# Optimization experiments

Hardware: AMD Instinct MI355X
Metric: run time of the kernel (lower is better)

## Reference

```python
import jax, jax.numpy as jnp
import numpy as np
import math

B, C, A, W, H = 8, 128, 16, 64, 64


def setup_inputs() -> dict:
    key = jax.random.key(0)
    ks = jax.random.split(key, 7)
    s_in = 1.0 / math.sqrt(C)
    return {
        "x": jax.random.normal(ks[0], (B, C, W, H), dtype=jnp.float32),
        "Wq": jax.random.normal(ks[1], (A, C), dtype=jnp.float32) * s_in,
        "bq": jnp.zeros((A,), dtype=jnp.float32),
        "Wk": jax.random.normal(ks[2], (A, C), dtype=jnp.float32) * s_in,
        "bk": jnp.zeros((A,), dtype=jnp.float32),
        "Wv": jax.random.normal(ks[3], (C, C), dtype=jnp.float32) * s_in,
        "bv": jnp.zeros((C,), dtype=jnp.float32),
    }


def reference(x, Wq, bq, Wk, bk, Wv, bv):
    # 1x1 convs == per-pixel linear projections
    q = jnp.einsum('ac,bcwh->bawh', Wq, x) + bq[None, :, None, None]  # [B,A,W,H]
    k = jnp.einsum('ac,bcwh->bawh', Wk, x) + bk[None, :, None, None]  # [B,A,W,H]
    v = jnp.einsum('vc,bcwh->bvwh', Wv, x) + bv[None, :, None, None]  # [B,C,W,H]

    scale = 1.0 / math.sqrt(q.shape[1])
    # full spatial attention: [B, W, H, W, H]
    attn = jnp.einsum('bawh,baWH->bwhWH', q, k)
    b, w, h, _, _ = attn.shape
    attn = jax.nn.softmax(attn.reshape(b, w, h, -1) * scale, axis=-1)
    attn = attn.reshape(b, w, h, w, h)
    out = jnp.einsum('bwhWH,bvWH->bvwh', attn, v)  # [B,C,W,H]
    return out
```

## Files before the change

kernel.cpp:

```cpp
#include <hip/hip_runtime.h>
#include <math.h>

#define BB 8
#define CC 128
#define NN 4096

typedef _Float16 f16;
typedef _Float16 f16x4v __attribute__((ext_vector_type(4)));
typedef _Float16 f16x8 __attribute__((ext_vector_type(8)));
typedef float f32x16 __attribute__((ext_vector_type(16)));

#if __has_builtin(__builtin_amdgcn_exp2f)
#define EXP2(x) __builtin_amdgcn_exp2f(x)
#else
#define EXP2(x) __expf((x)*0.69314718056f)
#endif

#define QSCALE 0.360673760222f
#define SHIFT  5.770780163555f

#define WF_BYTES 65536

__global__ __launch_bounds__(256)
void prep_kernel(const float* __restrict__ Wq, const float* __restrict__ bq,
                 const float* __restrict__ Wk, const float* __restrict__ bk,
                 const float* __restrict__ Wv, const float* __restrict__ bv,
                 f16* __restrict__ Wf, float* __restrict__ biasS)
{
    const int tg = blockIdx.x*256 + threadIdx.x;
    if (tg < 2560) {
        const int mt = tg >> 9, ks = (tg >> 6) & 7, l = tg & 63;
        const int n32 = l & 31, h = l >> 5;
        const int r = mt*32 + n32;
        f16x8 v8;
        #pragma unroll
        for (int i = 0; i < 8; i++) {
            int c = ks*16 + 8*h + i;
            float wv_;
            if (r < 16)      wv_ = QSCALE * Wq[r*CC + c];
            else if (r < 32) wv_ = Wk[(r-16)*CC + c];
            else             wv_ = Wv[(r-32)*CC + c];
            v8[i] = (f16)wv_;
        }
        *(f16x8*)&Wf[(size_t)tg*8] = v8;
    }
    if (blockIdx.x == 0 && threadIdx.x < 160) {
        int r = threadIdx.x;
        biasS[r] = r < 16 ? QSCALE*bq[r] : (r < 32 ? bk[r-16] : bv[r-32]);
    }
}

__global__ __launch_bounds__(256)
void proj_kernel(const float* __restrict__ x, const f16* __restrict__ Wf,
                 const float* __restrict__ biasS,
                 f16* __restrict__ Qt, f16* __restrict__ Kt, f16* __restrict__ Vf)
{
    __shared__ __align__(16) f16 Vl[CC*140];

    const int tid  = threadIdx.x;
    const int lane = tid & 63;
    const int wv   = tid >> 6;
    const int b    = blockIdx.x & 7;
    const int pt   = blockIdx.x >> 3;
    const int n32  = lane & 31;
    const int half = lane >> 5;
    const int p    = pt*128 + wv*32 + n32;

    const float* xp = x + (size_t)b*CC*NN + p;
    f16x8 xf[8];
    #pragma unroll
    for (int ks = 0; ks < 8; ks++) {
        float xv[8];
        #pragma unroll
        for (int i = 0; i < 8; i++) xv[i] = xp[(size_t)(ks*16 + 8*half + i)*NN];
        #pragma unroll
        for (int i = 0; i < 8; i++) xf[ks][i] = (f16)xv[i];
    }

    f32x16 acc[5];
    #pragma unroll
    for (int mt = 0; mt < 5; mt++) acc[mt] = (f32x16)0.0f;
    #pragma unroll
    for (int ks = 0; ks < 8; ks++) {
        #pragma unroll
        for (int mt = 0; mt < 5; mt++) {
            f16x8 wfr = *(const f16x8*)&Wf[((size_t)(mt*8 + ks)*64 + lane)*8];
            acc[mt] = __builtin_amdgcn_mfma_f32_32x32x16_f16(wfr, xf[ks], acc[mt], 0, 0, 0);
        }
    }

    #pragma unroll
    for (int mt = 0; mt < 5; mt++) {
        #pragma unroll
        for (int q = 0; q < 4; q++) {
            float4 b4 = *(const float4*)&biasS[mt*32 + q*8 + 4*half];
            acc[mt][q*4+0] += b4.x; acc[mt][q*4+1] += b4.y;
            acc[mt][q*4+2] += b4.z; acc[mt][q*4+3] += b4.w;
        }
    }

    {
        size_t qkoff = ((size_t)b*NN + p)*16;
        f16x4v s0, s1, s2, s3;
        #pragma unroll
        for (int i = 0; i < 4; i++) {
            s0[i] = (f16)acc[0][i];    s1[i] = (f16)acc[0][4+i];
            s2[i] = (f16)acc[0][8+i];  s3[i] = (f16)acc[0][12+i];
        }
        *(f16x4v*)&Qt[qkoff + 4*half]     = s0;
        *(f16x4v*)&Qt[qkoff + 8 + 4*half] = s1;
        *(f16x4v*)&Kt[qkoff + 4*half]     = s2;
        *(f16x4v*)&Kt[qkoff + 8 + 4*half] = s3;
    }

    #pragma unroll
    for (int mt = 1; mt < 5; mt++) {
        #pragma unroll
        for (int g = 0; g < 16; g++) {
            int c = (mt-1)*32 + (g & 3) + 8*(g >> 2) + 4*half;
            Vl[c*140 + wv*32 + n32] = (f16)acc[mt][g];
        }
    }
    __syncthreads();

    #pragma unroll
    for (int pass = 0; pass < 8; pass++) {
        int item = pass*256 + tid;
        int l    = item & 63;
        int f    = (item >> 6) & 15;
        int ktl  = item >> 10;
        int kc   = f >> 2, ct = f & 3;
        int li   = l & 31, h2 = l >> 5;
        const f16* src = &Vl[(ct*32 + li)*140 + ktl*64 + kc*16 + 4*h2];
        f16x4v lo = *(const f16x4v*)&src[0];
        f16x4v hi = *(const f16x4v*)&src[8];
        f16x8 v8;
        #pragma unroll
        for (int i = 0; i < 4; i++) { v8[i] = lo[i]; v8[4+i] = hi[i]; }
        int ktg = pt*2 + ktl;
        *(f16x8*)&Vf[((((size_t)b*64 + ktg)*16 + f)*64 + l)*8] = v8;
    }
}

__global__ __launch_bounds__(256, 2)
void attn_kernel(const f16* __restrict__ Qt, const f16* __restrict__ Kt,
                 const f16* __restrict__ Vf, float* __restrict__ out)
{
    __shared__ __align__(16) unsigned char lds_raw[52480];

    const int tid  = threadIdx.x;
    const int lane = tid & 63;
    const int wv   = tid >> 6;
    const int b    = blockIdx.x & 7;
    const int qt   = blockIdx.x >> 3;
    const int q0   = qt*64;
    const int n32  = lane & 31;
    const int half = lane >> 5;

    const f16* vb = Vf + (size_t)b*64*16*512;
    const f16* kb = Kt + (size_t)b*NN*16;
    const f16x8 qfA = *(const f16x8*)&Qt[((size_t)b*NN + q0 + n32)*16 + half*8];
    const f16x8 qfB = *(const f16x8*)&Qt[((size_t)b*NN + q0 + 32 + n32)*16 + half*8];

    f32x16 ofA[4], ofB[4];
    #pragma unroll
    for (int ct = 0; ct < 4; ct++) { ofA[ct] = (f32x16)0.0f; ofB[ct] = (f32x16)0.0f; }
    float psA[4] = {0,0,0,0}, psB[4] = {0,0,0,0};

    f16x8 kf0 = *(const f16x8*)&kb[((size_t)wv*64 + n32)*16 + half*8];
    f16x8 kf1 = *(const f16x8*)&kb[((size_t)wv*64 + 32 + n32)*16 + half*8];

    for (int kt = wv; kt < NN/64; kt += 4) {
        const int ktn = (kt + 4 < NN/64) ? kt + 4 : kt;
        f16x8 kf0n = *(const f16x8*)&kb[((size_t)ktn*64 + n32)*16 + half*8];
        f16x8 kf1n = *(const f16x8*)&kb[((size_t)ktn*64 + 32 + n32)*16 + half*8];

        f32x16 St0 = __builtin_amdgcn_mfma_f32_32x32x16_f16(kf0, qfA, (f32x16)(-SHIFT), 0, 0, 0);
        f32x16 St1 = __builtin_amdgcn_mfma_f32_32x32x16_f16(kf1, qfA, (f32x16)(-SHIFT), 0, 0, 0);
        f32x16 St2 = __builtin_amdgcn_mfma_f32_32x32x16_f16(kf0, qfB, (f32x16)(-SHIFT), 0, 0, 0);
        f32x16 St3 = __builtin_amdgcn_mfma_f32_32x32x16_f16(kf1, qfB, (f32x16)(-SHIFT), 0, 0, 0);

        f16x8 pfA[4], pfB[4];
        #pragma unroll
        for (int g = 0; g < 16; g++) {
            float e0 = EXP2(St0[g]); psA[g & 3] += e0; pfA[(g >> 3)][g & 7]     = (f16)e0;
            float e1 = EXP2(St1[g]); psA[g & 3] += e1; pfA[2 + (g >> 3)][g & 7] = (f16)e1;
            float e2 = EXP2(St2[g]); psB[g & 3] += e2; pfB[(g >> 3)][g & 7]     = (f16)e2;
            float e3 = EXP2(St3[g]); psB[g & 3] += e3; pfB[2 + (g >> 3)][g & 7] = (f16)e3;
        }

        const f16* vt = vb + (size_t)kt*8192;
        #pragma unroll
        for (int kc = 0; kc < 4; kc++) {
            #pragma unroll
            for (int ct = 0; ct < 4; ct++) {
                f16x8 vfr = *(const f16x8*)&vt[((kc*4 + ct)*64 + lane)*8];
                ofA[ct] = __builtin_amdgcn_mfma_f32_32x32x16_f16(pfA[kc], vfr, ofA[ct], 0, 0, 0);
                ofB[ct] = __builtin_amdgcn_mfma_f32_32x32x16_f16(pfB[kc], vfr, ofB[ct], 0, 0, 0);
            }
        }
        kf0 = kf0n; kf1 = kf1n;
    }

    float lsA = (psA[0] + psA[1]) + (psA[2] + psA[3]);
    float lsB = (psB[0] + psB[1]) + (psB[2] + psB[3]);
    lsA += __shfl_xor(lsA, 32);
    lsB += __shfl_xor(lsB, 32);

    __syncthreads();
    if (wv != 0) {
        unsigned char* base = lds_raw + (size_t)(wv-1)*17408 + (size_t)lane*272;
        #pragma unroll
        for (int ct = 0; ct < 4; ct++) {
            #pragma unroll
            for (int h = 0; h < 2; h++) {
                f16x8 ta, tb;
                #pragma unroll
                for (int j = 0; j < 8; j++) { ta[j] = (f16)ofA[ct][h*8+j]; tb[j] = (f16)ofB[ct][h*8+j]; }
                *(f16x8*)(base + ct*32 + h*16)       = ta;
                *(f16x8*)(base + 128 + ct*32 + h*16) = tb;
            }
        }
        *(float*)(base + 256) = lsA;
        *(float*)(base + 260) = lsB;
    }
    __syncthreads();
    if (wv == 0) {
        #pragma unroll
        for (int s2 = 0; s2 < 3; s2++) {
            unsigned char* base = lds_raw + (size_t)s2*17408 + (size_t)lane*272;
            #pragma unroll
            for (int ct = 0; ct < 4; ct++) {
                #pragma unroll
                for (int h = 0; h < 2; h++) {
                    f16x8 ta = *(const f16x8*)(base + ct*32 + h*16);
                    f16x8 tb = *(const f16x8*)(base + 128 + ct*32 + h*16);
                    #pragma unroll
                    for (int j = 0; j < 8; j++) { ofA[ct][h*8+j] += (float)ta[j]; ofB[ct][h*8+j] += (float)tb[j]; }
                }
            }
            lsA += *(const float*)(base + 256);
            lsB += *(const float*)(base + 260);
        }
        float* ls_inv = (float*)(lds_raw + 52224);
        if (lane < 32) { ls_inv[lane] = 1.f / lsA; ls_inv[32 + lane] = 1.f / lsB; }
        float invA[16], invB[16];
        #pragma unroll
        for (int g = 0; g < 16; g++) {
            int row = (g & 3) + 8*(g >> 2) + 4*half;
            invA[g] = ls_inv[row];
            invB[g] = ls_inv[32 + row];
        }
        float* Tb = (float*)lds_raw;
        #pragma unroll
        for (int ct = 0; ct < 4; ct++) {
            #pragma unroll
            for (int g = 0; g < 16; g++) {
                int row = (g & 3) + 8*(g >> 2) + 4*half;
                Tb[(ct*32 + n32)*68 + row]      = ofA[ct][g] * invA[g];
                Tb[(ct*32 + n32)*68 + 32 + row] = ofB[ct][g] * invB[g];
            }
        }
    }
    __syncthreads();
    {
        const float* Tb = (const float*)lds_raw;
        #pragma unroll
        for (int it = 0; it < 8; it++) {
            int idx = it*256 + tid;
            int c = idx >> 4, qq = idx & 15;
            *(float4*)&out[((size_t)b*CC + c)*NN + q0 + qq*4] =
                *(const float4*)&Tb[c*68 + qq*4];
        }
    }
}

extern "C" void kernel_launch(void* const* d_in, const int* in_sizes, int n_in,
                              void* d_out, int out_size, void* d_ws, size_t ws_size,
                              hipStream_t stream) {
    const float* x  = (const float*)d_in[0];
    const float* Wq = (const float*)d_in[1];
    const float* bq = (const float*)d_in[2];
    const float* Wk = (const float*)d_in[3];
    const float* bk = (const float*)d_in[4];
    const float* Wv = (const float*)d_in[5];
    const float* bv = (const float*)d_in[6];
    float* out = (float*)d_out;

    f16* Qw = (f16*)d_ws;
    f16* Kw = Qw + (size_t)BB*NN*16;
    f16* Vw = Kw + (size_t)BB*NN*16;
    unsigned char* tail = (unsigned char*)d_out + (size_t)out_size*4 - WF_BYTES;
    f16*   Wf    = (f16*)tail;
    float* biasS = (float*)(tail + 49152);

    hipLaunchKernelGGL(prep_kernel, dim3(10), dim3(256), 0, stream,
                       Wq, bq, Wk, bk, Wv, bv, Wf, biasS);
    hipLaunchKernelGGL(proj_kernel, dim3(256), dim3(256), 0, stream,
                       x, Wf, biasS, Qw, Kw, Vw);
    hipLaunchKernelGGL(attn_kernel, dim3(512), dim3(256), 0, stream,
                       Qw, Kw, Vw, out);
}
```

Measured before the change: 154.8 us.

## Halve attention query tile to 32 rows, double grid, prefetch V fragments into registers

The attention kernel now processes 32 queries per block instead of 64 and launches 1024 blocks, which halves per-wave accumulator registers and LDS use and doubles the number of blocks. V fragments for the next key tile are prefetched into registers while the current tile's MFMAs run, hiding global load latency. The projection kernel's x loads become nontemporal. The cost is that each block now reads K and V for only half as many queries, so total K/V traffic doubles.

```diff
diff --git a/kernel.cpp b/kernel.cpp
--- a/kernel.cpp
+++ b/kernel.cpp
@@ -72,7 +72,8 @@
     for (int ks = 0; ks < 8; ks++) {
         float xv[8];
         #pragma unroll
-        for (int i = 0; i < 8; i++) xv[i] = xp[(size_t)(ks*16 + 8*half + i)*NN];
+        for (int i = 0; i < 8; i++)
+            xv[i] = __builtin_nontemporal_load(&xp[(size_t)(ks*16 + 8*half + i)*NN]);
         #pragma unroll
         for (int i = 0; i < 8; i++) xf[ks][i] = (f16)xv[i];
     }
@@ -146,119 +147,112 @@
 void attn_kernel(const f16* __restrict__ Qt, const f16* __restrict__ Kt,
                  const f16* __restrict__ Vf, float* __restrict__ out)
 {
-    __shared__ __align__(16) unsigned char lds_raw[52480];
+    __shared__ __align__(16) unsigned char lds_raw[27776];
 
     const int tid  = threadIdx.x;
     const int lane = tid & 63;
     const int wv   = tid >> 6;
     const int b    = blockIdx.x & 7;
     const int qt   = blockIdx.x >> 3;
-    const int q0   = qt*64;
+    const int q0   = qt*32;
     const int n32  = lane & 31;
     const int half = lane >> 5;
 
     const f16* vb = Vf + (size_t)b*64*16*512;
     const f16* kb = Kt + (size_t)b*NN*16;
-    const f16x8 qfA = *(const f16x8*)&Qt[((size_t)b*NN + q0 + n32)*16 + half*8];
-    const f16x8 qfB = *(const f16x8*)&Qt[((size_t)b*NN + q0 + 32 + n32)*16 + half*8];
-
-    f32x16 ofA[4], ofB[4];
-    #pragma unroll
-    for (int ct = 0; ct < 4; ct++) { ofA[ct] = (f32x16)0.0f; ofB[ct] = (f32x16)0.0f; }
-    float psA[4] = {0,0,0,0}, psB[4] = {0,0,0,0};
+    const f16x8 qf = *(const f16x8*)&Qt[((size_t)b*NN + q0 + n32)*16 + half*8];
+
+    f32x16 of[4];
+    #pragma unroll
+    for (int ct = 0; ct < 4; ct++) of[ct] = (f32x16)0.0f;
+    float ps[4] = {0.f, 0.f, 0.f, 0.f};
 
     f16x8 kf0 = *(const f16x8*)&kb[((size_t)wv*64 + n32)*16 + half*8];
     f16x8 kf1 = *(const f16x8*)&kb[((size_t)wv*64 + 32 + n32)*16 + half*8];
+    f16x8 vpf[16];
+    {
+        const f16* vt = vb + (size_t)wv*8192;
+        #pragma unroll
+        for (int i = 0; i < 16; i++)
+            vpf[i] = *(const f16x8*)&vt[((size_t)i*64 + lane)*8];
+    }
 
     for (int kt = wv; kt < NN/64; kt += 4) {
         const int ktn = (kt + 4 < NN/64) ? kt + 4 : kt;
         f16x8 kf0n = *(const f16x8*)&kb[((size_t)ktn*64 + n32)*16 + half*8];
         f16x8 kf1n = *(const f16x8*)&kb[((size_t)ktn*64 + 32 + n32)*16 + half*8];
 
-        f32x16 St0 = __builtin_amdgcn_mfma_f32_32x32x16_f16(kf0, qfA, (f32x16)(-SHIFT), 0, 0, 0);
-        f32x16 St1 = __builtin_amdgcn_mfma_f32_32x32x16_f16(kf1, qfA, (f32x16)(-SHIFT), 0, 0, 0);
-        f32x16 St2 = __builtin_amdgcn_mfma_f32_32x32x16_f16(kf0, qfB, (f32x16)(-SHIFT), 0, 0, 0);
-        f32x16 St3 = __builtin_amdgcn_mfma_f32_32x32x16_f16(kf1, qfB, (f32x16)(-SHIFT), 0, 0, 0);
-
-        f16x8 pfA[4], pfB[4];
+        f32x16 St0 = __builtin_amdgcn_mfma_f32_32x32x16_f16(kf0, qf, (f32x16)(-SHIFT), 0, 0, 0);
+        f32x16 St1 = __builtin_amdgcn_mfma_f32_32x32x16_f16(kf1, qf, (f32x16)(-SHIFT), 0, 0, 0);
+
+        f16x8 pf[4];
         #pragma unroll
         for (int g = 0; g < 16; g++) {
-            float e0 = EXP2(St0[g]); psA[g & 3] += e0; pfA[(g >> 3)][g & 7]     = (f16)e0;
-            float e1 = EXP2(St1[g]); psA[g & 3] += e1; pfA[2 + (g >> 3)][g & 7] = (f16)e1;
-            float e2 = EXP2(St2[g]); psB[g & 3] += e2; pfB[(g >> 3)][g & 7]     = (f16)e2;
-            float e3 = EXP2(St3[g]); psB[g & 3] += e3; pfB[2 + (g >> 3)][g & 7] = (f16)e3;
-        }
-
-        const f16* vt = vb + (size_t)kt*8192;
+            float e0 = EXP2(St0[g]); ps[g & 3] += e0; pf[(g >> 3)][g & 7]     = (f16)e0;
+            float e1 = EXP2(St1[g]); ps[g & 3] += e1; pf[2 + (g >> 3)][g & 7] = (f16)e1;
+        }
+
+        const f16* vtn = vb + (size_t)ktn*8192;
         #pragma unroll
         for (int kc = 0; kc < 4; kc++) {
             #pragma unroll
             for (int ct = 0; ct < 4; ct++) {
-                f16x8 vfr = *(const f16x8*)&vt[((kc*4 + ct)*64 + lane)*8];
-                ofA[ct] = __builtin_amdgcn_mfma_f32_32x32x16_f16(pfA[kc], vfr, ofA[ct], 0, 0, 0);
-                ofB[ct] = __builtin_amdgcn_mfma_f32_32x32x16_f16(pfB[kc], vfr, ofB[ct], 0, 0, 0);
+                const int i = kc*4 + ct;
+                f16x8 vc = vpf[i];
+                vpf[i] = *(const f16x8*)&vtn[((size_t)i*64 + lane)*8];
+                of[ct] = __builtin_amdgcn_mfma_f32_32x32x16_f16(pf[kc], vc, of[ct], 0, 0, 0);
             }
         }
         kf0 = kf0n; kf1 = kf1n;
     }
 
-    float lsA = (psA[0] + psA[1]) + (psA[2] + psA[3]);
-    float lsB = (psB[0] + psB[1]) + (psB[2] + psB[3]);
-    lsA += __shfl_xor(lsA, 32);
-    lsB += __shfl_xor(lsB, 32);
+    float ls = (ps[0] + ps[1]) + (ps[2] + ps[3]);
+    ls += __shfl_xor(ls, 32);
 
     __syncthreads();
     if (wv != 0) {
-        unsigned char* base = lds_raw + (size_t)(wv-1)*17408 + (size_t)lane*272;
+        unsigned char* base = lds_raw + (size_t)(wv-1)*9216 + (size_t)lane*144;
         #pragma unroll
         for (int ct = 0; ct < 4; ct++) {
             #pragma unroll
             for (int h = 0; h < 2; h++) {
-                f16x8 ta, tb;
+                f16x8 t;
                 #pragma unroll
-                for (int j = 0; j < 8; j++) { ta[j] = (f16)ofA[ct][h*8+j]; tb[j] = (f16)ofB[ct][h*8+j]; }
-                *(f16x8*)(base + ct*32 + h*16)       = ta;
-                *(f16x8*)(base + 128 + ct*32 + h*16) = tb;
-            }
-        }
-        *(float*)(base + 256) = lsA;
-        *(float*)(base + 260) = lsB;
+                for (int jj = 0; jj < 8; jj++) t[jj] = (f16)of[ct][h*8+jj];
+                *(f16x8*)(base + ct*32 + h*16) = t;
+            }
+        }
+        *(float*)(base + 128) = ls;
     }
     __syncthreads();
     if (wv == 0) {
         #pragma unroll
         for (int s2 = 0; s2 < 3; s2++) {
-            unsigned char* base = lds_raw + (size_t)s2*17408 + (size_t)lane*272;
+            unsigned char* base = lds_raw + (size_t)s2*9216 + (size_t)lane*144;
             #pragma unroll
             for (int ct = 0; ct < 4; ct++) {
                 #pragma unroll
                 for (int h = 0; h < 2; h++) {
-                    f16x8 ta = *(const f16x8*)(base + ct*32 + h*16);
-                    f16x8 tb = *(const f16x8*)(base + 128 + ct*32 + h*16);
+                    f16x8 t = *(const f16x8*)(base + ct*32 + h*16);
                     #pragma unroll
-                    for (int j = 0; j < 8; j++) { ofA[ct][h*8+j] += (float)ta[j]; ofB[ct][h*8+j] += (float)tb[j]; }
+                    for (int jj = 0; jj < 8; jj++) of[ct][h*8+jj] += (float)t[jj];
                 }
             }
-            lsA += *(const float*)(base + 256);
-            lsB += *(const float*)(base + 260);
-        }
-        float* ls_inv = (float*)(lds_raw + 52224);
-        if (lane < 32) { ls_inv[lane] = 1.f / lsA; ls_inv[32 + lane] = 1.f / lsB; }
-        float invA[16], invB[16];
-        #pragma unroll
-        for (int g = 0; g < 16; g++) {
-            int row = (g & 3) + 8*(g >> 2) + 4*half;
-            invA[g] = ls_inv[row];
-            invB[g] = ls_inv[32 + row];
-        }
+            ls += *(const float*)(base + 128);
+        }
+        float* ls_inv = (float*)(lds_raw + 27648);
+        if (lane < 32) ls_inv[lane] = 1.f / ls;
+        float invq[16];
+        #pragma unroll
+        for (int g = 0; g < 16; g++)
+            invq[g] = ls_inv[(g & 3) + 8*(g >> 2) + 4*half];
         float* Tb = (float*)lds_raw;
         #pragma unroll
         for (int ct = 0; ct < 4; ct++) {
             #pragma unroll
             for (int g = 0; g < 16; g++) {
                 int row = (g & 3) + 8*(g >> 2) + 4*half;
-                Tb[(ct*32 + n32)*68 + row]      = ofA[ct][g] * invA[g];
-                Tb[(ct*32 + n32)*68 + 32 + row] = ofB[ct][g] * invB[g];
+                Tb[(ct*32 + n32)*36 + row] = of[ct][g] * invq[g];
             }
         }
     }
@@ -266,11 +260,11 @@
     {
         const float* Tb = (const float*)lds_raw;
         #pragma unroll
-        for (int it = 0; it < 8; it++) {
+        for (int it = 0; it < 4; it++) {
             int idx = it*256 + tid;
-            int c = idx >> 4, qq = idx & 15;
+            int c = idx >> 3, qq = idx & 7;
             *(float4*)&out[((size_t)b*CC + c)*NN + q0 + qq*4] =
-                *(const float4*)&Tb[c*68 + qq*4];
+                *(const float4*)&Tb[c*36 + qq*4];
         }
     }
 }
@@ -298,6 +292,6 @@
                        Wq, bq, Wk, bk, Wv, bv, Wf, biasS);
     hipLaunchKernelGGL(proj_kernel, dim3(256), dim3(256), 0, stream,
                        x, Wf, biasS, Qw, Kw, Vw);
-    hipLaunchKernelGGL(attn_kernel, dim3(512), dim3(256), 0, stream,
+    hipLaunchKernelGGL(attn_kernel, dim3(1024), dim3(256), 0, stream,
                        Qw, Kw, Vw, out);
 }
```

Result: faster. 138.8 us (-10.3%).
